# Performance work log

Measured on AMD Instinct MI355X. Metric: run time of the kernel, lower is better.

## Reference

```python
import jax, jax.numpy as jnp
import numpy as np

N, E, R = 50000, 400000, 500
X_SIZE = 100
G_SIZE = 100
HID = 64
OUT = 64
HEADS = 2
ALPHA = 0.5
NEG_SLOPE = 0.01  # nn.LeakyReLU default and attention slope
EPS = 1e-12       # F.normalize eps


def _l2norm(x, axis):
    return x / jnp.maximum(jnp.linalg.norm(x, axis=axis, keepdims=True), EPS)


def _xavier(key, shape, gain=1.414):
    fan_in, fan_out = shape[-1], int(np.prod(shape[:-1]))
    std = gain * np.sqrt(2.0 / (fan_in + fan_out))
    return jax.random.normal(key, shape, dtype=jnp.float32) * std


def _att_layer(h, g, row, col, etype, W, b, att, out_size):
    # h: [N, D_h], g: [R, D_g], W: [heads*out, 2*D_h+D_g], att: [1, heads, out]
    n = h.shape[0]
    h_ijk = jnp.concatenate([h[row], h[col], g[etype]], axis=1)      # [E, 2D_h+D_g]
    c_ijk = (h_ijk @ W.T + b).reshape(-1, HEADS, out_size)           # [E, H, O]
    a = jnp.sum(att * c_ijk, axis=2, keepdims=True)                  # [E, H, 1]
    e = jnp.exp(jax.nn.leaky_relu(a, NEG_SLOPE))                     # unnormalized (matches torch exp w/o max-sub)
    denom = jax.ops.segment_sum(e, row, num_segments=n)              # [N, H, 1]
    alpha = e / denom[row]
    # self-edge zeros contribute nothing; segment_sum over num_segments=n is equivalent
    return jax.ops.segment_sum(alpha * c_ijk, col, num_segments=n)   # [N, H, O]


def setup_inputs() -> dict:
    key = jax.random.key(0)
    ks = jax.random.split(key, 20)
    x = jax.random.normal(ks[0], (N, X_SIZE), dtype=jnp.float32)
    g = jax.random.normal(ks[1], (R, G_SIZE), dtype=jnp.float32)
    edge_idx = jax.random.randint(ks[2], (2, E), 0, N)
    edge_type = jax.random.randint(ks[3], (E,), 0, R)
    d1 = 2 * X_SIZE + G_SIZE
    d2 = 2 * HID * HEADS + G_SIZE
    inp = {
        "x": x, "g": g, "edge_idx": edge_idx, "edge_type": edge_type,
        "W1i": _xavier(ks[4], (HEADS * HID, d1)), "b1i": jnp.zeros((HEADS * HID,), jnp.float32),
        "a1i": _xavier(ks[5], (1, HEADS, HID)),
        "W1o": _xavier(ks[6], (HEADS * HID, d1)), "b1o": jnp.zeros((HEADS * HID,), jnp.float32),
        "a1o": _xavier(ks[7], (1, HEADS, HID)),
        "W2i": _xavier(ks[8], (HEADS * OUT, d2)), "b2i": jnp.zeros((HEADS * OUT,), jnp.float32),
        "a2i": _xavier(ks[9], (1, HEADS, OUT)),
        "W2o": _xavier(ks[10], (HEADS * OUT, d2)), "b2o": jnp.zeros((HEADS * OUT,), jnp.float32),
        "a2o": _xavier(ks[11], (1, HEADS, OUT)),
        "We": _xavier(ks[12], (HID, X_SIZE)), "be": jnp.zeros((HID,), jnp.float32),
        "Wr": _xavier(ks[13], (HEADS * HID, G_SIZE)), "br": jnp.zeros((HEADS * HID,), jnp.float32),
    }
    return inp


def reference(x, g, edge_idx, edge_type, W1i, b1i, a1i, W1o, b1o, a1o,
              W2i, b2i, a2i, W2o, b2o, a2o, We, be, Wr, br):
    # x = F.normalize(x, dim=1).detach()
    xn = jax.lax.stop_gradient(_l2norm(x, axis=1))
    row, col = edge_idx[0], edge_idx[1]

    h_in = _att_layer(xn, g, row, col, edge_type, W1i, b1i, a1i, HID)
    h_out = _att_layer(xn, g, col, row, edge_type, W1o, b1o, a1o, HID)
    h = jax.nn.leaky_relu(ALPHA * h_in + (1.0 - ALPHA) * h_out, NEG_SLOPE)
    h = _l2norm(h, axis=2)                                # [N, H, HID]
    h = h.transpose(0, 1, 2).reshape(N, HEADS * HID)      # concat heads

    h_in = _att_layer(h, g, row, col, edge_type, W2i, b2i, a2i, OUT)
    h_out = _att_layer(h, g, col, row, edge_type, W2o, b2o, a2o, OUT)
    h = jax.nn.leaky_relu(ALPHA * h_in + (1.0 - ALPHA) * h_out, NEG_SLOPE)
    h = _l2norm(h, axis=2)                                # [N, H, OUT]

    # EntityLayer: Linear(x)[:, None, :] + h  (requires HID == OUT)
    h_prime = (xn @ We.T + be)[:, None, :] + h            # [N, H, OUT]
    h_prime = h_prime.reshape(N, HEADS * OUT)
    h_prime = _l2norm(h_prime, axis=1)                    # (torch dim=2 bug -> last dim)
    # _merge_heads stores mean but returns input unchanged

    g_prime = g @ Wr.T + br                               # [R, HEADS*HID]
    return h_prime, g_prime
```

## Files before the change

kernel.cpp:

```cpp
#include <hip/hip_runtime.h>

typedef unsigned short u16;
typedef unsigned int u32;
typedef short short8v __attribute__((ext_vector_type(8)));
typedef float float4v __attribute__((ext_vector_type(4)));

#define N_NODES 50000
#define E_EDGES 400000
#define R_REL   500
#define NKEYS   100000
#define SCAN_B  98
#define SEG     ((size_t)N_NODES * 128)

__device__ __forceinline__ float bl(u32 u){ return __uint_as_float(u << 16); }
__device__ __forceinline__ float bh(u32 u){ return __uint_as_float(u & 0xffff0000u); }
__device__ __forceinline__ u16 f2b(float f){
    u32 u = __float_as_uint(f);
    return (u16)((u + 0x7fffu + ((u >> 16) & 1u)) >> 16);
}
__device__ __forceinline__ u32 pk2(float a, float b){ return (u32)f2b(a) | ((u32)f2b(b) << 16); }
__device__ __forceinline__ float lrelu(float x){ return x > 0.f ? x : 0.01f * x; }

__global__ void k_norm_x(const float* __restrict__ x, u16* __restrict__ xnb){
    int wid = threadIdx.x >> 6, l = threadIdx.x & 63;
    int n = blockIdx.x * 4 + wid;
    if (n >= N_NODES) return;
    float v0 = x[(size_t)n * 100 + l];
    float v1 = (l + 64 < 100) ? x[(size_t)n * 100 + 64 + l] : 0.f;
    float ss = v0 * v0 + v1 * v1;
    #pragma unroll
    for (int m = 32; m; m >>= 1) ss += __shfl_xor(ss, m);
    float s = 1.f / fmaxf(sqrtf(ss), 1e-12f);
    xnb[(size_t)n * 128 + l] = f2b(v0 * s);
    xnb[(size_t)n * 128 + 64 + l] = (l + 64 < 100) ? f2b(v1 * s) : (u16)0;
}

__global__ void k_build_wcat(const float* __restrict__ W1i, const float* __restrict__ W1o,
                             const float* __restrict__ W2i, const float* __restrict__ W2o,
                             const float* __restrict__ We,
                             const float* __restrict__ a1i, const float* __restrict__ a1o,
                             const float* __restrict__ a2i, const float* __restrict__ a2o,
                             u16* __restrict__ wc1, u16* __restrict__ wc2,
                             float* __restrict__ attcat){
    int idx = blockIdx.x * blockDim.x + threadIdx.x;
    if (idx < 576 * 128){
        int r = idx >> 7, k = idx & 127;
        float v = 0.f;
        if (r < 512){
            int seg = r >> 7, rr = r & 127;
            const float* W = (seg < 2) ? W1i : W1o;
            int off = (seg & 1) ? 100 : 0;
            if (k < 100) v = W[(size_t)rr * 300 + off + k];
        } else {
            int rr = r - 512;
            if (k < 100) v = We[(size_t)rr * 100 + k];
        }
        wc1[idx] = f2b(v);
    } else if (idx < 576 * 128 + 512 * 128){
        int j = idx - 576 * 128;
        int r = j >> 7, k = j & 127;
        int seg = r >> 7, rr = r & 127;
        const float* W = (seg < 2) ? W2i : W2o;
        int off = (seg & 1) ? 128 : 0;
        wc2[j] = f2b(W[(size_t)rr * 356 + off + k]);
    } else if (idx < 576 * 128 + 512 * 128 + 1024){
        int j = idx - (576 * 128 + 512 * 128);
        int s = j >> 9, cc = j & 511;
        const float* a = s ? ((cc < 256) ? a2i : a2o) : ((cc < 256) ? a1i : a1o);
        attcat[j] = a[cc & 127];
    }
}

__global__ void k_pg(const float* __restrict__ g,
                     const float* __restrict__ W1i, const float* __restrict__ W1o,
                     const float* __restrict__ W2i, const float* __restrict__ W2o,
                     const float* __restrict__ b1i, const float* __restrict__ b1o,
                     const float* __restrict__ b2i, const float* __restrict__ b2o,
                     const float* __restrict__ a1i, const float* __restrict__ a1o,
                     const float* __restrict__ a2i, const float* __restrict__ a2o,
                     float* __restrict__ Pg, float* __restrict__ qg){
    int bid = blockIdx.x;
    int r = bid >> 2, t = bid & 3;
    const float *W, *b, *att; int ld, off;
    if (t == 0){ W = W1i; ld = 300; off = 200; b = b1i; att = a1i; }
    else if (t == 1){ W = W1o; ld = 300; off = 200; b = b1o; att = a1o; }
    else if (t == 2){ W = W2i; ld = 356; off = 256; b = b2i; att = a2i; }
    else { W = W2o; ld = 356; off = 256; b = b2o; att = a2o; }
    __shared__ float gs[100];
    __shared__ float red[128];
    int j = threadIdx.x;
    if (j < 100) gs[j] = g[(size_t)r * 100 + j];
    __syncthreads();
    float acc = b[j];
    #pragma unroll 4
    for (int k = 0; k < 100; ++k) acc += gs[k] * W[(size_t)j * ld + off + k];
    Pg[((size_t)t * R_REL + r) * 128 + j] = acc;
    red[j] = att[j] * acc;
    __syncthreads();
    if (j < 2){
        float s = 0.f;
        for (int k = 0; k < 64; ++k) s += red[j * 64 + k];
        qg[((size_t)t * R_REL + r) * 2 + j] = s;
    }
}

__global__ void k_gprime(const float* __restrict__ g, const float* __restrict__ Wr,
                         const float* __restrict__ br, float* __restrict__ out){
    int r = blockIdx.x, j = threadIdx.x;
    __shared__ float gs[100];
    if (j < 100) gs[j] = g[(size_t)r * 100 + j];
    __syncthreads();
    float acc = br[j];
    #pragma unroll 4
    for (int k = 0; k < 100; ++k) acc += gs[k] * Wr[(size_t)j * 100 + k];
    out[(size_t)N_NODES * 128 + (size_t)r * 128 + j] = acc;
}

__launch_bounds__(256)
__global__ void k_gemm(const u16* __restrict__ A, const u16* __restrict__ W,
                       const float* __restrict__ attcat,
                       u16* __restrict__ NPt, float* __restrict__ q, int M, int NN){
    __shared__ __align__(16) char lds[4 * 16 * 272];
    int l = threadIdx.x & 63, w = threadIdx.x >> 6;
    int rb = blockIdx.x * 64 + w * 16;
    int grp = blockIdx.y;
    int cb = grp * 128;
    int ncols = NN - cb; if (ncols > 128) ncols = 128;
    int tiles = ncols >> 4;
    int rowW = (ncols == 128) ? 128 : 64;
    int pitch = rowW * 2 + 16;
    char* lw = lds + w * 16 * pitch;

    int ar = rb + (l & 15); if (ar >= M) ar = M - 1;
    const u16* Ap = A + (size_t)ar * 128 + (l >> 4) * 8;
    short8v a0 = *(const short8v*)(Ap);
    short8v a1 = *(const short8v*)(Ap + 32);
    short8v a2 = *(const short8v*)(Ap + 64);
    short8v a3 = *(const short8v*)(Ap + 96);
    float qa[4] = {0.f, 0.f, 0.f, 0.f};
    bool doq = (cb < 512);
    int rloc0 = (l >> 4) * 4;
    for (int t = 0; t < tiles; ++t){
        int cc = cb + t * 16 + (l & 15);
        const u16* Wp = W + (size_t)cc * 128 + (l >> 4) * 8;
        short8v b0 = *(const short8v*)(Wp);
        short8v b1 = *(const short8v*)(Wp + 32);
        short8v b2 = *(const short8v*)(Wp + 64);
        short8v b3 = *(const short8v*)(Wp + 96);
        float4v acc = {0.f, 0.f, 0.f, 0.f};
        acc = __builtin_amdgcn_mfma_f32_16x16x32_bf16(a0, b0, acc, 0, 0, 0);
        acc = __builtin_amdgcn_mfma_f32_16x16x32_bf16(a1, b1, acc, 0, 0, 0);
        acc = __builtin_amdgcn_mfma_f32_16x16x32_bf16(a2, b2, acc, 0, 0, 0);
        acc = __builtin_amdgcn_mfma_f32_16x16x32_bf16(a3, b3, acc, 0, 0, 0);
        int lcol = t * 16 + (l & 15);
        #pragma unroll
        for (int r = 0; r < 4; ++r)
            *(u16*)(lw + (size_t)(rloc0 + r) * pitch + lcol * 2) = f2b(acc[r]);
        if (doq){
            float av = attcat[cc];
            #pragma unroll
            for (int r = 0; r < 4; ++r) qa[r] += av * acc[r];
            if ((t & 3) == 3){
                int g = (cb >> 6) + (t >> 2);
                #pragma unroll
                for (int r = 0; r < 4; ++r){
                    float s = qa[r];
                    s += __shfl_xor(s, 1); s += __shfl_xor(s, 2);
                    s += __shfl_xor(s, 4); s += __shfl_xor(s, 8);
                    if ((l & 15) == 0){
                        int rr = rb + rloc0 + r;
                        if (rr < M) q[(size_t)rr * 8 + g] = s;
                    }
                    qa[r] = 0.f;
                }
            }
        }
    }
    __syncthreads();
    u16* gb = (rowW == 128) ? (NPt + (size_t)grp * SEG + (size_t)rb * 128)
                            : (NPt + 4 * SEG + (size_t)rb * 64);
    int chunks = (rowW == 128) ? 4 : 2;
    for (int i = 0; i < chunks; ++i){
        int u = i * 512 + l * 8;
        int rloc = (rowW == 128) ? (u >> 7) : (u >> 6);
        int c    = (rowW == 128) ? (u & 127) : (u & 63);
        if (rb + rloc < M){
            short8v v = *(const short8v*)(lw + (size_t)rloc * pitch + c * 2);
            *(short8v*)(gb + u) = v;
        }
    }
}

__global__ void k_hist(const int* __restrict__ ei, u32* __restrict__ cnt){
    int e = blockIdx.x * blockDim.x + threadIdx.x;
    if (e >= E_EDGES) return;
    atomicAdd(&cnt[ei[E_EDGES + e]], 1u);
    atomicAdd(&cnt[N_NODES + ei[e]], 1u);
}

__launch_bounds__(1024)
__global__ void k_scan1(const u32* __restrict__ cnt, u32* __restrict__ off, u32* __restrict__ bsum){
    __shared__ u32 sh[1024];
    int t = threadIdx.x, b = blockIdx.x, idx = b * 1024 + t;
    u32 v = cnt[idx];
    sh[t] = v; __syncthreads();
    #pragma unroll
    for (int d = 1; d < 1024; d <<= 1){
        u32 add = (t >= d) ? sh[t - d] : 0;
        __syncthreads();
        sh[t] += add;
        __syncthreads();
    }
    off[idx] = sh[t] - v;
    if (t == 1023) bsum[b] = sh[1023];
}

__global__ void k_scan2(u32* __restrict__ bsum){
    if (threadIdx.x == 0){
        u32 run = 0;
        for (int i = 0; i < SCAN_B; ++i){ u32 t = bsum[i]; bsum[i] = run; run += t; }
    }
}

__launch_bounds__(1024)
__global__ void k_scan3(u32* __restrict__ off, const u32* __restrict__ bsum){
    int idx = blockIdx.x * 1024 + threadIdx.x;
    off[idx] += bsum[blockIdx.x];
}

__global__ void k_pos(const int* __restrict__ ei, const int* __restrict__ ety,
                      u32* __restrict__ cur,
                      u32* __restrict__ Pso, u32* __restrict__ Pss){
    int e = blockIdx.x * blockDim.x + threadIdx.x;
    if (e >= E_EDGES) return;
    u32 row = (u32)ei[e], col = (u32)ei[E_EDGES + e];
    u32 etb = (u32)ety[e] << 20;
    u32 pI = atomicAdd(&cur[col], 1u);
    Pso[pI] = row | etb;  Pss[pI] = col;
    u32 pO = atomicAdd(&cur[N_NODES + row], 1u);
    Pso[pO] = col | etb;  Pss[pO] = row;
}

__global__ void k_edgeA(const u32* __restrict__ Pso, const u32* __restrict__ Pss,
                        const float* __restrict__ q,
                        const float* __restrict__ qgI, const float* __restrict__ qgO,
                        float2* __restrict__ exI, float2* __restrict__ exO){
    int p = blockIdx.x * blockDim.x + threadIdx.x;
    if (p >= 2 * E_EDGES) return;
    u32 so = Pso[p], self = Pss[p];
    u32 oth = so & 0xFFFFF, et = so >> 20;
    u32 row, col;
    if (p < E_EDGES){ row = oth; col = self; } else { row = self; col = oth; }
    const float* qr = q + (size_t)row * 8;
    const float* qc = q + (size_t)col * 8;
    float2 ri, ro;
    ri.x = expf(lrelu(qr[0] + qc[2] + qgI[(size_t)et * 2 + 0]));
    ri.y = expf(lrelu(qr[1] + qc[3] + qgI[(size_t)et * 2 + 1]));
    ro.x = expf(lrelu(qc[4] + qr[6] + qgO[(size_t)et * 2 + 0]));
    ro.y = expf(lrelu(qc[5] + qr[7] + qgO[(size_t)et * 2 + 1]));
    exI[p] = ri;
    exO[p] = ro;
}

__global__ void k_denom(const u32* __restrict__ off,
                        const float2* __restrict__ exI, const float2* __restrict__ exO,
                        float* __restrict__ rdI, float* __restrict__ rdO){
    int n = blockIdx.x * blockDim.x + threadIdx.x;
    if (n >= N_NODES) return;
    float s0 = 0.f, s1 = 0.f;
    for (u32 p = off[N_NODES + n]; p < off[N_NODES + n + 1]; ++p){
        float2 v = exI[p]; s0 += v.x; s1 += v.y;
    }
    rdI[(size_t)n * 2 + 0] = (s0 > 0.f) ? 1.f / s0 : 0.f;
    rdI[(size_t)n * 2 + 1] = (s1 > 0.f) ? 1.f / s1 : 0.f;
    float t0 = 0.f, t1 = 0.f;
    for (u32 p = off[n]; p < off[n + 1]; ++p){
        float2 v = exO[p]; t0 += v.x; t1 += v.y;
    }
    rdO[(size_t)n * 2 + 0] = (t0 > 0.f) ? 1.f / t0 : 0.f;
    rdO[(size_t)n * 2 + 1] = (t1 > 0.f) ? 1.f / t1 : 0.f;
}

__launch_bounds__(256)
__global__ void k_agg(const u32* __restrict__ off,
                      const u32* __restrict__ Pso,
                      const float2* __restrict__ exI, const float2* __restrict__ exO,
                      const u16* __restrict__ NPt,
                      const float* __restrict__ PgI, const float* __restrict__ PgO,
                      const float* __restrict__ rdI, const float* __restrict__ rdO,
                      int final_stage,
                      const u16* __restrict__ NPt1, const float* __restrict__ be,
                      u16* __restrict__ h1b, float* __restrict__ out){
    int wid = threadIdx.x >> 6, l = threadIdx.x & 63;
    int n = blockIdx.x * 4 + wid;
    if (n >= N_NODES) return;
    int h = l >> 5, d0 = l * 2;
    const u16* PaI = NPt;
    const u16* PbI = NPt + SEG;
    const u16* PaO = NPt + 2 * SEG;
    const u16* PbO = NPt + 3 * SEG;
    u32 pbi = *(const u32*)(PbI + (size_t)n * 128 + d0);
    u32 pbo = *(const u32*)(PbO + (size_t)n * 128 + d0);

    float a0 = 0.f, a1 = 0.f, sai = 0.f;
    {
        u32 s0 = off[n], deg = off[n + 1] - s0;
        for (u32 base = 0; base < deg; base += 64){
            u32 k = base + (u32)l;
            u32 so = 0u; float w0 = 0.f, w1 = 0.f;
            if (k < deg){
                u32 idx = s0 + k;
                so = __builtin_nontemporal_load(Pso + idx);
                const float* ep = (const float*)exI + (size_t)idx * 2;
                float e0 = __builtin_nontemporal_load(ep);
                float e1 = __builtin_nontemporal_load(ep + 1);
                u32 oth = so & 0xFFFFFu;
                float2 rd2 = *(const float2*)(rdI + (size_t)oth * 2);
                w0 = e0 * rd2.x; w1 = e1 * rd2.y;
            }
            int cnt = (int)((deg - base < 64u) ? (deg - base) : 64u);
            for (int c = 0; c < cnt; c += 8){
                float wj[8]; u32 pa[8]; float2 gv[8];
                #pragma unroll
                for (int j = 0; j < 8; ++j){
                    u32 s = __shfl(so, c + j);
                    float v0 = __shfl(w0, c + j);
                    float v1 = __shfl(w1, c + j);
                    u32 oth = s & 0xFFFFFu, et = s >> 20;
                    pa[j] = *(const u32*)(PaI + (size_t)oth * 128 + d0);
                    gv[j] = *(const float2*)(PgI + (size_t)et * 128 + d0);
                    wj[j] = h ? v1 : v0;
                }
                #pragma unroll
                for (int j = 0; j < 8; ++j){
                    a0 += wj[j] * (bl(pa[j]) + gv[j].x);
                    a1 += wj[j] * (bh(pa[j]) + gv[j].y);
                    sai += wj[j];
                }
            }
        }
    }
    a0 += sai * bl(pbi);
    a1 += sai * bh(pbi);

    float b0 = 0.f, b1 = 0.f, sao = 0.f;
    {
        u32 s0 = off[N_NODES + n], deg = off[N_NODES + n + 1] - s0;
        for (u32 base = 0; base < deg; base += 64){
            u32 k = base + (u32)l;
            u32 so = 0u; float w0 = 0.f, w1 = 0.f;
            if (k < deg){
                u32 idx = s0 + k;
                so = __builtin_nontemporal_load(Pso + idx);
                const float* ep = (const float*)exO + (size_t)idx * 2;
                float e0 = __builtin_nontemporal_load(ep);
                float e1 = __builtin_nontemporal_load(ep + 1);
                u32 oth = so & 0xFFFFFu;
                float2 rd2 = *(const float2*)(rdO + (size_t)oth * 2);
                w0 = e0 * rd2.x; w1 = e1 * rd2.y;
            }
            int cnt = (int)((deg - base < 64u) ? (deg - base) : 64u);
            for (int c = 0; c < cnt; c += 8){
                float wj[8]; u32 pa[8]; float2 gv[8];
                #pragma unroll
                for (int j = 0; j < 8; ++j){
                    u32 s = __shfl(so, c + j);
                    float v0 = __shfl(w0, c + j);
                    float v1 = __shfl(w1, c + j);
                    u32 oth = s & 0xFFFFFu, et = s >> 20;
                    pa[j] = *(const u32*)(PaO + (size_t)oth * 128 + d0);
                    gv[j] = *(const float2*)(PgO + (size_t)et * 128 + d0);
                    wj[j] = h ? v1 : v0;
                }
                #pragma unroll
                for (int j = 0; j < 8; ++j){
                    b0 += wj[j] * (bl(pa[j]) + gv[j].x);
                    b1 += wj[j] * (bh(pa[j]) + gv[j].y);
                    sao += wj[j];
                }
            }
        }
    }
    b0 += sao * bl(pbo);
    b1 += sao * bh(pbo);

    float vx = lrelu(0.5f * (a0 + b0));
    float vy = lrelu(0.5f * (a1 + b1));
    float ss = vx * vx + vy * vy;
    #pragma unroll
    for (int m = 16; m; m >>= 1) ss += __shfl_xor(ss, m);
    float s2 = 1.f / fmaxf(sqrtf(ss), 1e-12f);
    if (!final_stage){
        *(u32*)(h1b + (size_t)n * 128 + d0) = pk2(vx * s2, vy * s2);
    } else {
        float h20 = vx * s2, h21 = vy * s2;
        int o0 = d0 & 63;
        u32 ue = *(const u32*)(NPt1 + 4 * SEG + (size_t)n * 64 + o0);
        float hp0 = bl(ue) + be[o0] + h20;
        float hp1 = bh(ue) + be[o0 + 1] + h21;
        float st = hp0 * hp0 + hp1 * hp1;
        #pragma unroll
        for (int m = 32; m; m >>= 1) st += __shfl_xor(st, m);
        float s = 1.f / fmaxf(sqrtf(st), 1e-12f);
        float2 o; o.x = hp0 * s; o.y = hp1 * s;
        *(float2*)(out + (size_t)n * 128 + d0) = o;
    }
}

extern "C" void kernel_launch(void* const* d_in, const int* in_sizes, int n_in,
                              void* d_out, int out_size, void* d_ws, size_t ws_size,
                              hipStream_t stream){
    const float* x   = (const float*)d_in[0];
    const float* g   = (const float*)d_in[1];
    const int*   ei  = (const int*)d_in[2];
    const int*   ety = (const int*)d_in[3];
    const float* W1i = (const float*)d_in[4];
    const float* b1i = (const float*)d_in[5];
    const float* a1i = (const float*)d_in[6];
    const float* W1o = (const float*)d_in[7];
    const float* b1o = (const float*)d_in[8];
    const float* a1o = (const float*)d_in[9];
    const float* W2i = (const float*)d_in[10];
    const float* b2i = (const float*)d_in[11];
    const float* a2i = (const float*)d_in[12];
    const float* W2o = (const float*)d_in[13];
    const float* b2o = (const float*)d_in[14];
    const float* a2o = (const float*)d_in[15];
    const float* We  = (const float*)d_in[16];
    const float* be  = (const float*)d_in[17];
    const float* Wr  = (const float*)d_in[18];
    const float* br  = (const float*)d_in[19];
    float* out = (float*)d_out;

    char* ws = (char*)d_ws;
    size_t off_b = 0;
    auto carve = [&](size_t bytes) -> char* {
        char* p = ws + off_b;
        off_b += (bytes + 255) & ~(size_t)255;
        return p;
    };
    u16*    xnb   = (u16*)carve((size_t)N_NODES * 128 * 2);
    u16*    wc1   = (u16*)carve((size_t)576 * 128 * 2);
    u16*    wc2   = (u16*)carve((size_t)512 * 128 * 2);
    float*  attct = (float*)carve((size_t)1024 * 4);
    u16*    NPt1  = (u16*)carve((SEG * 4 + (size_t)N_NODES * 64) * 2);
    u16*    NPt2  = (u16*)carve(SEG * 4 * 2);
    u16*    h1b   = (u16*)carve((size_t)N_NODES * 128 * 2);
    float*  q     = (float*)carve((size_t)N_NODES * 8 * 4);
    float*  Pg    = (float*)carve((size_t)4 * R_REL * 128 * 4);
    float*  qg    = (float*)carve((size_t)4 * R_REL * 2 * 4);
    u32*    cnt   = (u32*)carve((size_t)SCAN_B * 1024 * 4);
    u32*    offA  = (u32*)carve((size_t)SCAN_B * 1024 * 4);
    u32*    cur   = (u32*)carve((size_t)NKEYS * 4);
    u32*    bsum  = (u32*)carve((size_t)SCAN_B * 4);
    u32*    Pso   = (u32*)carve((size_t)2 * E_EDGES * 4);
    u32*    Pss   = (u32*)carve((size_t)2 * E_EDGES * 4);
    float2* exI   = (float2*)carve((size_t)2 * E_EDGES * 8);
    float2* exO   = (float2*)carve((size_t)2 * E_EDGES * 8);
    float*  rdI   = (float*)carve((size_t)N_NODES * 2 * 4);
    float*  rdO   = (float*)carve((size_t)N_NODES * 2 * 4);

    hipMemsetAsync(cnt, 0, (size_t)SCAN_B * 1024 * 4, stream);
    k_hist<<<1563, 256, 0, stream>>>(ei, cnt);
    k_scan1<<<SCAN_B, 1024, 0, stream>>>(cnt, offA, bsum);
    k_scan2<<<1, 64, 0, stream>>>(bsum);
    k_scan3<<<SCAN_B, 1024, 0, stream>>>(offA, bsum);
    hipMemcpyAsync(cur, offA, (size_t)NKEYS * 4, hipMemcpyDeviceToDevice, stream);
    k_pos<<<1563, 256, 0, stream>>>(ei, ety, cur, Pso, Pss);

    k_norm_x<<<12500, 256, 0, stream>>>(x, xnb);
    k_build_wcat<<<548, 256, 0, stream>>>(W1i, W1o, W2i, W2o, We,
                                          a1i, a1o, a2i, a2o, wc1, wc2, attct);
    k_pg<<<2000, 128, 0, stream>>>(g, W1i, W1o, W2i, W2o, b1i, b1o, b2i, b2o,
                                   a1i, a1o, a2i, a2o, Pg, qg);
    k_gprime<<<500, 128, 0, stream>>>(g, Wr, br, out);

    k_gemm<<<dim3(782, 5), 256, 0, stream>>>(xnb, wc1, attct, NPt1, q, N_NODES, 576);
    k_edgeA<<<3125, 256, 0, stream>>>(Pso, Pss, q, qg, qg + R_REL * 2, exI, exO);
    k_denom<<<196, 256, 0, stream>>>(offA, exI, exO, rdI, rdO);
    k_agg<<<12500, 256, 0, stream>>>(offA, Pso, exI, exO, NPt1, Pg, Pg + R_REL * 128,
                                     rdI, rdO, 0, NPt1, be, h1b, out);

    k_gemm<<<dim3(782, 4), 256, 0, stream>>>(h1b, wc2, attct + 512, NPt2, q, N_NODES, 512);
    k_edgeA<<<3125, 256, 0, stream>>>(Pso, Pss, q, qg + 2 * R_REL * 2, qg + 3 * R_REL * 2,
                                      exI, exO);
    k_denom<<<196, 256, 0, stream>>>(offA, exI, exO, rdI, rdO);
    k_agg<<<12500, 256, 0, stream>>>(offA, Pso, exI, exO, NPt2, Pg + 2 * R_REL * 128,
                                     Pg + 3 * R_REL * 128, rdI, rdO, 1, NPt1, be, h1b, out);
}
```

Baseline: 425.5 us.

## Split in/out edge aggregation across separate wavefronts and combine via LDS

The aggregation kernel now gives each node two wavefronts, one walking incoming edges and one walking outgoing edges, instead of one wavefront doing both loops in sequence. The partial results meet through shared memory after a block barrier, and the in-direction wave finishes the nonlinearity, normalisation and output. This doubles wave-level parallelism and memory-level parallelism on the latency-bound gather. In exchange it adds a __syncthreads and LDS traffic, and the grid doubles while each block still holds 256 threads but covers only 2 nodes.

```diff
diff --git a/kernel.cpp b/kernel.cpp
--- a/kernel.cpp
+++ b/kernel.cpp
@@ -291,119 +291,85 @@
                       int final_stage,
                       const u16* __restrict__ NPt1, const float* __restrict__ be,
                       u16* __restrict__ h1b, float* __restrict__ out){
-    int wid = threadIdx.x >> 6, l = threadIdx.x & 63;
-    int n = blockIdx.x * 4 + wid;
-    if (n >= N_NODES) return;
+    __shared__ float2 comb[2][64];
+    int tid = threadIdx.x;
+    int wv = tid >> 6, l = tid & 63;
+    int slot = wv >> 1, dir = wv & 1;
+    int n = blockIdx.x * 2 + slot;
     int h = l >> 5, d0 = l * 2;
-    const u16* PaI = NPt;
-    const u16* PbI = NPt + SEG;
-    const u16* PaO = NPt + 2 * SEG;
-    const u16* PbO = NPt + 3 * SEG;
-    u32 pbi = *(const u32*)(PbI + (size_t)n * 128 + d0);
-    u32 pbo = *(const u32*)(PbO + (size_t)n * 128 + d0);
-
-    float a0 = 0.f, a1 = 0.f, sai = 0.f;
-    {
-        u32 s0 = off[n], deg = off[n + 1] - s0;
-        for (u32 base = 0; base < deg; base += 64){
-            u32 k = base + (u32)l;
-            u32 so = 0u; float w0 = 0.f, w1 = 0.f;
-            if (k < deg){
-                u32 idx = s0 + k;
-                so = __builtin_nontemporal_load(Pso + idx);
-                const float* ep = (const float*)exI + (size_t)idx * 2;
-                float e0 = __builtin_nontemporal_load(ep);
-                float e1 = __builtin_nontemporal_load(ep + 1);
-                u32 oth = so & 0xFFFFFu;
-                float2 rd2 = *(const float2*)(rdI + (size_t)oth * 2);
-                w0 = e0 * rd2.x; w1 = e1 * rd2.y;
+
+    const u16* Pa  = NPt + (dir ? 2 * SEG : 0);
+    const u16* Pb  = NPt + (dir ? 3 * SEG : SEG);
+    const float2* ex = dir ? exO : exI;
+    const float*  rd = dir ? rdO : rdI;
+    const float*  Pgd = dir ? PgO : PgI;
+    int key = dir ? (N_NODES + n) : n;
+
+    u32 s0 = off[key], deg = off[key + 1] - s0;
+    float r0 = 0.f, r1 = 0.f, sw = 0.f;
+    for (u32 base = 0; base < deg; base += 64){
+        u32 k = base + (u32)l;
+        u32 so = 0u; float w0 = 0.f, w1 = 0.f;
+        if (k < deg){
+            u32 idx = s0 + k;
+            so = __builtin_nontemporal_load(Pso + idx);
+            const float* ep = (const float*)ex + (size_t)idx * 2;
+            float e0 = __builtin_nontemporal_load(ep);
+            float e1 = __builtin_nontemporal_load(ep + 1);
+            u32 oth = so & 0xFFFFFu;
+            float2 rd2 = *(const float2*)(rd + (size_t)oth * 2);
+            w0 = e0 * rd2.x; w1 = e1 * rd2.y;
+        }
+        int cnt = (int)((deg - base < 64u) ? (deg - base) : 64u);
+        for (int c = 0; c < cnt; c += 8){
+            float wj[8]; u32 pa[8]; float2 gv[8];
+            #pragma unroll
+            for (int j = 0; j < 8; ++j){
+                u32 s = __shfl(so, c + j);
+                float v0 = __shfl(w0, c + j);
+                float v1 = __shfl(w1, c + j);
+                u32 oth = s & 0xFFFFFu, et = s >> 20;
+                pa[j] = *(const u32*)(Pa + (size_t)oth * 128 + d0);
+                gv[j] = *(const float2*)(Pgd + (size_t)et * 128 + d0);
+                wj[j] = h ? v1 : v0;
             }
-            int cnt = (int)((deg - base < 64u) ? (deg - base) : 64u);
-            for (int c = 0; c < cnt; c += 8){
-                float wj[8]; u32 pa[8]; float2 gv[8];
-                #pragma unroll
-                for (int j = 0; j < 8; ++j){
-                    u32 s = __shfl(so, c + j);
-                    float v0 = __shfl(w0, c + j);
-                    float v1 = __shfl(w1, c + j);
-                    u32 oth = s & 0xFFFFFu, et = s >> 20;
-                    pa[j] = *(const u32*)(PaI + (size_t)oth * 128 + d0);
-                    gv[j] = *(const float2*)(PgI + (size_t)et * 128 + d0);
-                    wj[j] = h ? v1 : v0;
-                }
-                #pragma unroll
-                for (int j = 0; j < 8; ++j){
-                    a0 += wj[j] * (bl(pa[j]) + gv[j].x);
-                    a1 += wj[j] * (bh(pa[j]) + gv[j].y);
-                    sai += wj[j];
-                }
+            #pragma unroll
+            for (int j = 0; j < 8; ++j){
+                r0 += wj[j] * (bl(pa[j]) + gv[j].x);
+                r1 += wj[j] * (bh(pa[j]) + gv[j].y);
+                sw += wj[j];
             }
         }
     }
-    a0 += sai * bl(pbi);
-    a1 += sai * bh(pbi);
-
-    float b0 = 0.f, b1 = 0.f, sao = 0.f;
-    {
-        u32 s0 = off[N_NODES + n], deg = off[N_NODES + n + 1] - s0;
-        for (u32 base = 0; base < deg; base += 64){
-            u32 k = base + (u32)l;
-            u32 so = 0u; float w0 = 0.f, w1 = 0.f;
-            if (k < deg){
-                u32 idx = s0 + k;
-                so = __builtin_nontemporal_load(Pso + idx);
-                const float* ep = (const float*)exO + (size_t)idx * 2;
-                float e0 = __builtin_nontemporal_load(ep);
-                float e1 = __builtin_nontemporal_load(ep + 1);
-                u32 oth = so & 0xFFFFFu;
-                float2 rd2 = *(const float2*)(rdO + (size_t)oth * 2);
-                w0 = e0 * rd2.x; w1 = e1 * rd2.y;
-            }
-            int cnt = (int)((deg - base < 64u) ? (deg - base) : 64u);
-            for (int c = 0; c < cnt; c += 8){
-                float wj[8]; u32 pa[8]; float2 gv[8];
-                #pragma unroll
-                for (int j = 0; j < 8; ++j){
-                    u32 s = __shfl(so, c + j);
-                    float v0 = __shfl(w0, c + j);
-                    float v1 = __shfl(w1, c + j);
-                    u32 oth = s & 0xFFFFFu, et = s >> 20;
-                    pa[j] = *(const u32*)(PaO + (size_t)oth * 128 + d0);
-                    gv[j] = *(const float2*)(PgO + (size_t)et * 128 + d0);
-                    wj[j] = h ? v1 : v0;
-                }
-                #pragma unroll
-                for (int j = 0; j < 8; ++j){
-                    b0 += wj[j] * (bl(pa[j]) + gv[j].x);
-                    b1 += wj[j] * (bh(pa[j]) + gv[j].y);
-                    sao += wj[j];
-                }
-            }
-        }
-    }
-    b0 += sao * bl(pbo);
-    b1 += sao * bh(pbo);
-
-    float vx = lrelu(0.5f * (a0 + b0));
-    float vy = lrelu(0.5f * (a1 + b1));
-    float ss = vx * vx + vy * vy;
-    #pragma unroll
-    for (int m = 16; m; m >>= 1) ss += __shfl_xor(ss, m);
-    float s2 = 1.f / fmaxf(sqrtf(ss), 1e-12f);
-    if (!final_stage){
-        *(u32*)(h1b + (size_t)n * 128 + d0) = pk2(vx * s2, vy * s2);
-    } else {
-        float h20 = vx * s2, h21 = vy * s2;
-        int o0 = d0 & 63;
-        u32 ue = *(const u32*)(NPt1 + 4 * SEG + (size_t)n * 64 + o0);
-        float hp0 = bl(ue) + be[o0] + h20;
-        float hp1 = bh(ue) + be[o0 + 1] + h21;
-        float st = hp0 * hp0 + hp1 * hp1;
+    u32 pb = *(const u32*)(Pb + (size_t)n * 128 + d0);
+    r0 += sw * bl(pb);
+    r1 += sw * bh(pb);
+
+    if (dir == 1){ comb[slot][l] = make_float2(r0, r1); }
+    __syncthreads();
+    if (dir == 0){
+        float2 o2 = comb[slot][l];
+        float vx = lrelu(0.5f * (r0 + o2.x));
+        float vy = lrelu(0.5f * (r1 + o2.y));
+        float ss = vx * vx + vy * vy;
         #pragma unroll
-        for (int m = 32; m; m >>= 1) st += __shfl_xor(st, m);
-        float s = 1.f / fmaxf(sqrtf(st), 1e-12f);
-        float2 o; o.x = hp0 * s; o.y = hp1 * s;
-        *(float2*)(out + (size_t)n * 128 + d0) = o;
+        for (int m = 16; m; m >>= 1) ss += __shfl_xor(ss, m);
+        float s2 = 1.f / fmaxf(sqrtf(ss), 1e-12f);
+        if (!final_stage){
+            *(u32*)(h1b + (size_t)n * 128 + d0) = pk2(vx * s2, vy * s2);
+        } else {
+            float h20 = vx * s2, h21 = vy * s2;
+            int o0 = d0 & 63;
+            u32 ue = *(const u32*)(NPt1 + 4 * SEG + (size_t)n * 64 + o0);
+            float hp0 = bl(ue) + be[o0] + h20;
+            float hp1 = bh(ue) + be[o0 + 1] + h21;
+            float st = hp0 * hp0 + hp1 * hp1;
+            #pragma unroll
+            for (int m = 32; m; m >>= 1) st += __shfl_xor(st, m);
+            float s = 1.f / fmaxf(sqrtf(st), 1e-12f);
+            float2 o; o.x = hp0 * s; o.y = hp1 * s;
+            *(float2*)(out + (size_t)n * 128 + d0) = o;
+        }
     }
 }
 
@@ -478,13 +444,13 @@
     k_gemm<<<dim3(782, 5), 256, 0, stream>>>(xnb, wc1, attct, NPt1, q, N_NODES, 576);
     k_edgeA<<<3125, 256, 0, stream>>>(Pso, Pss, q, qg, qg + R_REL * 2, exI, exO);
     k_denom<<<196, 256, 0, stream>>>(offA, exI, exO, rdI, rdO);
-    k_agg<<<12500, 256, 0, stream>>>(offA, Pso, exI, exO, NPt1, Pg, Pg + R_REL * 128,
+    k_agg<<<25000, 256, 0, stream>>>(offA, Pso, exI, exO, NPt1, Pg, Pg + R_REL * 128,
                                      rdI, rdO, 0, NPt1, be, h1b, out);
 
     k_gemm<<<dim3(782, 4), 256, 0, stream>>>(h1b, wc2, attct + 512, NPt2, q, N_NODES, 512);
     k_edgeA<<<3125, 256, 0, stream>>>(Pso, Pss, q, qg + 2 * R_REL * 2, qg + 3 * R_REL * 2,
                                       exI, exO);
     k_denom<<<196, 256, 0, stream>>>(offA, exI, exO, rdI, rdO);
-    k_agg<<<12500, 256, 0, stream>>>(offA, Pso, exI, exO, NPt2, Pg + 2 * R_REL * 128,
+    k_agg<<<25000, 256, 0, stream>>>(offA, Pso, exI, exO, NPt2, Pg + 2 * R_REL * 128,
                                      Pg + 3 * R_REL * 128, rdI, rdO, 1, NPt1, be, h1b, out);
 }
```

Measured after the change: 440.0 us. 1.03x slower.
